# Kernel tuning notes

Hardware: AMD Instinct MI355X
Metric: run time of the kernel (lower is better)

Reference implementation:

```python
import jax, jax.numpy as jnp
import numpy as np

BN = 1024      # B*N voxel groups
M = 32         # points per voxel
D_MODEL = 128
D_POINTS = 64


def _mlp(x, w1, b1, w2, b2):
    # Linear -> ReLU -> Linear (torch nn.Sequential equivalent)
    return jax.nn.relu(x @ w1 + b1) @ w2 + b2


def setup_inputs() -> dict:
    key = jax.random.key(0)
    ks = jax.random.split(key, 16)
    def lin(k, din, dout):
        return (jax.random.normal(k, (din, dout), jnp.float32) / np.sqrt(din)).astype(jnp.float32)
    inp = {}
    inp["pv_xyz"] = jax.random.normal(ks[0], (BN, M, 3), jnp.float32)
    inp["features"] = jax.random.normal(ks[1], (BN, M, D_POINTS), jnp.float32)
    i = 2
    for name, din in [("alpha", 3), ("beta", 3), ("delta", 3), ("epsilon", D_MODEL), ("omega", D_POINTS)]:
        inp[f"{name}_w1"] = lin(ks[i], din, D_MODEL); i += 1
        inp[f"{name}_b1"] = jnp.zeros((D_MODEL,), jnp.float32)
        inp[f"{name}_w2"] = lin(ks[i], D_MODEL, D_MODEL); i += 1
        inp[f"{name}_b2"] = jnp.zeros((D_MODEL,), jnp.float32)
    return inp


def reference(pv_xyz, features,
              alpha_w1, alpha_b1, alpha_w2, alpha_b2,
              beta_w1, beta_b1, beta_w2, beta_b2,
              delta_w1, delta_b1, delta_w2, delta_b2,
              epsilon_w1, epsilon_b1, epsilon_w2, epsilon_b2,
              omega_w1, omega_b1, omega_w2, omega_b2):
    # abs relative position: [BN, M, M, 3]
    dist = jnp.abs(pv_xyz[:, :, None, :] - pv_xyz[:, None, :, :])
    pij = _mlp(dist, delta_w1, delta_b1, delta_w2, delta_b2)          # [BN,M,M,D]
    q = _mlp(pv_xyz, alpha_w1, alpha_b1, alpha_w2, alpha_b2)          # [BN,M,D]
    k = _mlp(pv_xyz, beta_w1, beta_b1, beta_w2, beta_b2)              # [BN,M,D]
    v = _mlp(features, omega_w1, omega_b1, omega_w2, omega_b2)        # [BN,M,D]
    scale = jnp.float32(1.0 / np.sqrt(D_MODEL))
    w = _mlp((q[:, :, None, :] - k[:, None, :, :] + pij) * scale,
             epsilon_w1, epsilon_b1, epsilon_w2, epsilon_b2)          # [BN,M,M,D]
    wij = jax.nn.softmax(w, axis=-2)                                  # softmax over key axis
    # torch.einsum('bmmf,bmf->bmf', wij, v): repeated index -> diagonal of wij
    midx = jnp.arange(wij.shape[1])
    res = wij[:, midx, midx, :] * v                                   # [BN,M,D]
    return jnp.concatenate([res, features], axis=-1)                  # [BN,M,D+C]
```

## Files before the change

### kernel.cpp

```cpp
#include <hip/hip_runtime.h>
#include <hip/hip_bf16.h>
#include <cstdint>
#include <cstddef>


#define SCALE 0.08838834764831843f
#define LOG2E 1.4426950408889634f

typedef __bf16 bf16x8 __attribute__((ext_vector_type(8)));
typedef float f32x16 __attribute__((ext_vector_type(16)));
typedef unsigned int u32x2 __attribute__((ext_vector_type(2)));

__device__ __forceinline__ ushort f2b(float f){
  __hip_bfloat16 h = __float2bfloat16(f);
  return __builtin_bit_cast(ushort, h);
}
__device__ __forceinline__ float b2f(uint32_t s){
  union { uint32_t u; float f; } x; x.u = s << 16; return x.f;
}
__device__ __forceinline__ float blo(uint32_t u){
  union { uint32_t x; float f; } v; v.x = u << 16; return v.f;
}
__device__ __forceinline__ float bhi(uint32_t u){
  union { uint32_t x; float f; } v; v.x = u & 0xffff0000u; return v.f;
}
__device__ __forceinline__ uint32_t pk2(float a, float b){
  union { __hip_bfloat162 h2; uint32_t u; } x;
  x.h2.x = __float2bfloat16(a); x.h2.y = __float2bfloat16(b);
  return x.u;
}
__device__ __forceinline__ f32x16 MFMA(uint4 a, uint4 b, f32x16 c){
  return __builtin_amdgcn_mfma_f32_32x32x16_bf16(
      __builtin_bit_cast(bf16x8, a), __builtin_bit_cast(bf16x8, b), c, 0, 0, 0);
}

__device__ __forceinline__ uint2 pswap(uint32_t a, uint32_t b){
#if __has_builtin(__builtin_amdgcn_permlane32_swap)
  u32x2 r = __builtin_amdgcn_permlane32_swap(a, b, false, false);
  uint2 o; o.x = r[0]; o.y = r[1]; return o;
#else
  uint32_t am = (uint32_t)__shfl_xor((int)a, 32);
  uint32_t bm = (uint32_t)__shfl_xor((int)b, 32);
  bool hi = (threadIdx.x & 32) != 0;
  uint2 o; o.x = hi ? bm : a; o.y = hi ? b : am; return o;
#endif
}

__device__ __forceinline__ void packswap(const f32x16 c, uint4& f0, uint4& f1){
  uint32_t p01 = pk2(fmaxf(c[0],0.f),  fmaxf(c[1],0.f));
  uint32_t p23 = pk2(fmaxf(c[2],0.f),  fmaxf(c[3],0.f));
  uint32_t p45 = pk2(fmaxf(c[4],0.f),  fmaxf(c[5],0.f));
  uint32_t p67 = pk2(fmaxf(c[6],0.f),  fmaxf(c[7],0.f));
  uint32_t p89 = pk2(fmaxf(c[8],0.f),  fmaxf(c[9],0.f));
  uint32_t pab = pk2(fmaxf(c[10],0.f), fmaxf(c[11],0.f));
  uint32_t pcd = pk2(fmaxf(c[12],0.f), fmaxf(c[13],0.f));
  uint32_t pef = pk2(fmaxf(c[14],0.f), fmaxf(c[15],0.f));
  uint2 s0 = pswap(p01, p45), s1 = pswap(p23, p67);
  uint2 s2 = pswap(p89, pcd), s3 = pswap(pab, pef);
  f0.x = s0.x; f0.y = s1.x; f0.z = s0.y; f0.w = s1.y;
  f1.x = s2.x; f1.y = s3.x; f1.z = s2.y; f1.w = s3.y;
}

__global__ __launch_bounds__(256) void k_pre(
    const float* __restrict__ A2, const float* __restrict__ B2, const float* __restrict__ D2,
    const float* __restrict__ E1, const float* __restrict__ E2,
    const float* __restrict__ O1, const float* __restrict__ O2,
    const float* __restrict__ ab2, const float* __restrict__ bb2, const float* __restrict__ db2,
    const float* __restrict__ eb1,
    const float* __restrict__ D1, const float* __restrict__ db1,
    ushort* __restrict__ aep, ushort* __restrict__ bep, ushort* __restrict__ gtp,
    ushort* __restrict__ e2p, ushort* __restrict__ o2p, ushort* __restrict__ o1t,
    ushort* __restrict__ d1p, float* __restrict__ c0)
{
  const int bid = blockIdx.x, tid = threadIdx.x;
  if (bid < 192){
    const float* W = (bid < 64) ? A2 : (bid < 128) ? B2 : D2;
    ushort* dst    = (bid < 64) ? aep : (bid < 128) ? bep : gtp;
    int flat = (bid & 63)*256 + tid;
    int co = flat >> 10, rem = flat & 1023, h = rem >> 3, i = rem & 7;
    int r = co*8 + i;
    float acc = 0.f;
    for (int t = 0; t < 128; ++t) acc = fmaf(W[r*128 + t], E1[t*128 + h], acc);
    dst[(co*128 + h)*8 + i] = f2b(acc * SCALE);
  } else if (bid < 256){
    int flat = (bid - 192)*256 + tid;
    int co = flat >> 10, rem = flat & 1023, d = rem >> 3, i = rem & 7;
    e2p[(co*128 + d)*8 + i] = f2b(E2[(co*8 + i)*128 + d] * LOG2E);
  } else if (bid < 320){
    int flat = (bid - 256)*256 + tid;
    int co = flat >> 10, rem = flat & 1023, d = rem >> 3, i = rem & 7;
    o2p[(co*128 + d)*8 + i] = f2b(O2[(co*8 + i)*128 + d]);
  } else if (bid < 352){
    int flat = (bid - 320)*256 + tid;
    int fo = flat >> 10, rem = flat & 1023, o = rem >> 3, e = rem & 7;
    o1t[(fo*128 + o)*8 + e] = f2b(O1[(fo*8 + e)*128 + o]);
  } else if (bid < 360){
    int flat = (bid - 352)*256 + tid;
    int koct = flat >> 10, cd = (flat >> 3) & 127, e = flat & 7;
    float val = 0.f;
    if (koct == 0){
      if (e < 3) val = D1[e*128 + cd];
      else if (e == 3) val = db1[cd];
    }
    d1p[flat] = f2b(val);
  } else {
    if (tid < 128){
      float acc = 0.f;
      for (int t = 0; t < 128; ++t) acc = fmaf(ab2[t] - bb2[t] + db2[t], E1[t*128 + tid], acc);
      c0[tid] = acc * SCALE + eb1[tid];
    }
  }
}

__device__ __forceinline__ void gemm64x128(const ushort (*sa)[64][8], const ushort (*sw)[128][8],
                                           int w, int l31, int hl, int p0,
                                           const float* __restrict__ bias,
                                           ushort* __restrict__ dst)
{
  const int rw = w >> 1, ctb = (w & 1) * 2;
  f32x16 acc0, acc1;
#pragma unroll
  for (int r = 0; r < 16; ++r){ acc0[r] = 0.f; acc1[r] = 0.f; }
#pragma unroll
  for (int kk = 0; kk < 8; ++kk){
    uint4 a  = *(const uint4*)&sa[2*kk + hl][32*rw + l31][0];
    uint4 b0 = *(const uint4*)&sw[2*kk + hl][32*ctb + l31][0];
    uint4 b1 = *(const uint4*)&sw[2*kk + hl][32*(ctb+1) + l31][0];
    acc0 = MFMA(a, b0, acc0);
    acc1 = MFMA(a, b1, acc1);
  }
#pragma unroll
  for (int t = 0; t < 2; ++t){
    const f32x16 acc = t ? acc1 : acc0;
    const int d = 32*(ctb + t) + l31;
    const float bv = bias ? bias[d] : 0.f;
#pragma unroll
    for (int r = 0; r < 16; ++r){
      int row = 32*rw + (r & 3) + 8*(r >> 2) + 4*hl;
      dst[(size_t)(p0 + row)*128 + d] = f2b(acc[r] + bv);
    }
  }
}

__global__ __launch_bounds__(256, 2) void k_point(
    const float* __restrict__ pv, const float* __restrict__ feat,
    const float* __restrict__ A1, const float* __restrict__ ab1,
    const float* __restrict__ B1, const float* __restrict__ bb1,
    const float* __restrict__ ob1, const float* __restrict__ ob2,
    const float* __restrict__ c0,
    const uint4* __restrict__ aep, const uint4* __restrict__ bep,
    const uint4* __restrict__ o1t, const uint4* __restrict__ o2p,
    ushort* __restrict__ qe_ws, ushort* __restrict__ ke_ws, ushort* __restrict__ v_ws,
    float* __restrict__ out)
{
  __shared__ ushort sW[16][128][8];
  __shared__ ushort sA[16][64][8];
  __shared__ ushort sF[8][64][8];
  __shared__ float  sLw[3][128];
  __shared__ float  sLb[128];
  __shared__ float  sLb2[128];

  const int tid = threadIdx.x;
  const int p0  = blockIdx.x * 64;
  const int w = tid >> 6, lane = tid & 63, l31 = lane & 31, hl = lane >> 5;

  for (int idx = tid; idx < 64*16; idx += 256){
    int p = idx >> 4, k4 = idx & 15;
    float4 f = ((const float4*)(feat + (size_t)(p0 + p)*64))[k4];
    ((float4*)(out + (size_t)(p0 + p)*192 + 128))[k4] = f;
  }

  for (int idx = tid; idx < 2048; idx += 256) ((uint4*)sW)[idx] = aep[idx];
  for (int idx = tid; idx < 384; idx += 256) ((float*)sLw)[idx] = A1[idx];
  if (tid < 128) sLb[tid] = ab1[tid];
  __syncthreads();
  {
    int p = tid & 63, ob = tid >> 6;
    float x0 = pv[(size_t)(p0+p)*3+0], x1 = pv[(size_t)(p0+p)*3+1], x2 = pv[(size_t)(p0+p)*3+2];
#pragma unroll
    for (int it = 0; it < 4; ++it){
      int oct = ob + 4*it;
      float h[8];
#pragma unroll
      for (int e = 0; e < 8; ++e){
        int cd = oct*8 + e;
        float t = fmaf(x0, sLw[0][cd], fmaf(x1, sLw[1][cd], fmaf(x2, sLw[2][cd], sLb[cd])));
        h[e] = fmaxf(t, 0.f);
      }
      uint4 u; u.x = pk2(h[0],h[1]); u.y = pk2(h[2],h[3]); u.z = pk2(h[4],h[5]); u.w = pk2(h[6],h[7]);
      *(uint4*)&sA[oct][p][0] = u;
    }
  }
  __syncthreads();
  gemm64x128(sA, sW, w, l31, hl, p0, c0, qe_ws);
  __syncthreads();

  for (int idx = tid; idx < 2048; idx += 256) ((uint4*)sW)[idx] = bep[idx];
  for (int idx = tid; idx < 384; idx += 256) ((float*)sLw)[idx] = B1[idx];
  if (tid < 128) sLb[tid] = bb1[tid];
  __syncthreads();
  {
    int p = tid & 63, ob = tid >> 6;
    float x0 = pv[(size_t)(p0+p)*3+0], x1 = pv[(size_t)(p0+p)*3+1], x2 = pv[(size_t)(p0+p)*3+2];
#pragma unroll
    for (int it = 0; it < 4; ++it){
      int oct = ob + 4*it;
      float h[8];
#pragma unroll
      for (int e = 0; e < 8; ++e){
        int cd = oct*8 + e;
        float t = fmaf(x0, sLw[0][cd], fmaf(x1, sLw[1][cd], fmaf(x2, sLw[2][cd], sLb[cd])));
        h[e] = fmaxf(t, 0.f);
      }
      uint4 u; u.x = pk2(h[0],h[1]); u.y = pk2(h[2],h[3]); u.z = pk2(h[4],h[5]); u.w = pk2(h[6],h[7]);
      *(uint4*)&sA[oct][p][0] = u;
    }
  }
  __syncthreads();
  gemm64x128(sA, sW, w, l31, hl, p0, nullptr, ke_ws);
  __syncthreads();

  for (int idx = tid; idx < 512; idx += 256){
    int p = idx & 63, fo = idx >> 6;
    const float* fp = feat + (size_t)(p0 + p)*64 + 8*fo;
    float4 f0 = ((const float4*)fp)[0], f1 = ((const float4*)fp)[1];
    uint4 u; u.x = pk2(f0.x,f0.y); u.y = pk2(f0.z,f0.w); u.z = pk2(f1.x,f1.y); u.w = pk2(f1.z,f1.w);
    *(uint4*)&sF[fo][p][0] = u;
  }
  for (int idx = tid; idx < 1024; idx += 256) ((uint4*)sW)[idx] = o1t[idx];
  if (tid < 128) sLb[tid] = ob1[tid];
  __syncthreads();
  {
    f32x16 acc0, acc1;
#pragma unroll
    for (int r = 0; r < 16; ++r){ acc0[r] = 0.f; acc1[r] = 0.f; }
#pragma unroll
    for (int kk = 0; kk < 4; ++kk){
      uint4 a  = *(const uint4*)&sW[2*kk + hl][32*w + l31][0];
      uint4 b0 = *(const uint4*)&sF[2*kk + hl][l31][0];
      uint4 b1 = *(const uint4*)&sF[2*kk + hl][32 + l31][0];
      acc0 = MFMA(a, b0, acc0);
      acc1 = MFMA(a, b1, acc1);
    }
#pragma unroll
    for (int t = 0; t < 2; ++t){
      const f32x16 acc = t ? acc1 : acc0;
      const int pt = 32*t + l31;
#pragma unroll
      for (int q = 0; q < 4; ++q){
        int o0 = 32*w + 8*q + 4*hl;
        float z0 = fmaxf(acc[4*q+0] + sLb[o0+0], 0.f);
        float z1 = fmaxf(acc[4*q+1] + sLb[o0+1], 0.f);
        float z2 = fmaxf(acc[4*q+2] + sLb[o0+2], 0.f);
        float z3 = fmaxf(acc[4*q+3] + sLb[o0+3], 0.f);
        uint2 u; u.x = pk2(z0, z1); u.y = pk2(z2, z3);
        *(uint2*)&sA[4*w + q][pt][4*hl] = u;
      }
    }
  }
  __syncthreads();

  for (int idx = tid; idx < 2048; idx += 256) ((uint4*)sW)[idx] = o2p[idx];
  if (tid < 128) sLb2[tid] = ob2[tid];
  __syncthreads();
  {
    const int rw = w >> 1, ctb = (w & 1) * 2;
    f32x16 acc0, acc1;
#pragma unroll
    for (int r = 0; r < 16; ++r){ acc0[r] = 0.f; acc1[r] = 0.f; }
#pragma unroll
    for (int kk = 0; kk < 8; ++kk){
      uint4 a  = *(const uint4*)&sA[2*kk + hl][32*rw + l31][0];
      uint4 b0 = *(const uint4*)&sW[2*kk + hl][32*ctb + l31][0];
      uint4 b1 = *(const uint4*)&sW[2*kk + hl][32*(ctb+1) + l31][0];
      acc0 = MFMA(a, b0, acc0);
      acc1 = MFMA(a, b1, acc1);
    }
#pragma unroll
    for (int t = 0; t < 2; ++t){
      const f32x16 acc = t ? acc1 : acc0;
      const int d = 32*(ctb + t) + l31;
      const float bias = sLb2[d];
#pragma unroll
      for (int r = 0; r < 16; ++r){
        int row = 32*rw + (r & 3) + 8*(r >> 2) + 4*hl;
        v_ws[(size_t)(p0 + row)*128 + d] = f2b(acc[r] + bias);
      }
    }
  }
}

__global__ __launch_bounds__(256, 2) void k_main(
    const float* __restrict__ pv,
    const ushort* __restrict__ qe_ws, const ushort* __restrict__ ke_ws, const ushort* __restrict__ v_ws,
    const uint4* __restrict__ gtp, const uint4* __restrict__ e2p, const uint4* __restrict__ d1p,
    float* __restrict__ out)
{
  __shared__ uint4 sG[2048];
  __shared__ uint4 sE[2048];
  __shared__ uint2 sK[1024];
  __shared__ float sXYZ[32][3];

  const int tid = threadIdx.x;
  const int b = blockIdx.x;
  const int w = tid >> 6, lane = tid & 63, l31 = lane & 31, hl = lane >> 5;

  for (int idx = tid; idx < 2048; idx += 256){ sG[idx] = gtp[idx]; sE[idx] = e2p[idx]; }
  for (int idx = tid; idx < 1024; idx += 256){
    int j = idx & 31, rest = idx >> 5;
    int khl = rest & 1, slot = rest >> 1;
    int h0 = 32*(slot >> 2) + 8*(slot & 3) + 4*khl;
    sK[idx] = *(const uint2*)(ke_ws + (size_t)(b*32 + j)*128 + h0);
  }
  for (int idx = tid; idx < 96; idx += 256) ((float*)sXYZ)[idx] = pv[(size_t)b*96 + idx];

  uint4 wD[4];
#pragma unroll
  for (int t = 0; t < 4; ++t) wD[t] = d1p[hl*128 + 32*t + l31];
  f32x16 ZERO;
#pragma unroll
  for (int r = 0; r < 16; ++r) ZERO[r] = 0.f;
  __syncthreads();

  const float xj0 = sXYZ[l31][0], xj1 = sXYZ[l31][1], xj2 = sXYZ[l31][2];
  const ushort* qbase = qe_ws + (size_t)b*32*128;

#pragma unroll
  for (int pp = 0; pp < 4; ++pp){
    const int i0 = 8*w + 2*pp, i1 = i0 + 1;

    uint4 bDa, bDb;
    {
      float a0 = sXYZ[i0][0], a1 = sXYZ[i0][1], a2 = sXYZ[i0][2];
      float c0_ = sXYZ[i1][0], c1_ = sXYZ[i1][1], c2_ = sXYZ[i1][2];
      bDa.x = pk2(fabsf(a0-xj0), fabsf(a1-xj1)); bDa.y = pk2(fabsf(a2-xj2), 1.0f);
      bDa.z = 0u; bDa.w = 0u;
      bDb.x = pk2(fabsf(c0_-xj0), fabsf(c1_-xj1)); bDb.y = pk2(fabsf(c2_-xj2), 1.0f);
      bDb.z = 0u; bDb.w = 0u;
    }

    uint4 hdA[8], hdB[8];
#pragma unroll
    for (int t = 0; t < 4; ++t){
      f32x16 ca = MFMA(wD[t], bDa, ZERO);
      f32x16 cb = MFMA(wD[t], bDb, ZERO);
      packswap(ca, hdA[2*t], hdA[2*t+1]);
      packswap(cb, hdB[2*t], hdB[2*t+1]);
    }

    uint4 heA[8], heB[8];
#pragma unroll
    for (int t = 0; t < 4; ++t){
      f32x16 aA, aB;
#pragma unroll
      for (int q = 0; q < 4; ++q){
        uint2 kq = sK[((t*4 + q)*2 + hl)*32 + l31];
        uint2 qa = *(const uint2*)(qbase + (size_t)i0*128 + 32*t + 8*q + 4*hl);
        uint2 qb = *(const uint2*)(qbase + (size_t)i1*128 + 32*t + 8*q + 4*hl);
        float k0 = blo(kq.x), k1 = bhi(kq.x), k2 = blo(kq.y), k3 = bhi(kq.y);
        aA[4*q+0] = blo(qa.x) - k0; aA[4*q+1] = bhi(qa.x) - k1;
        aA[4*q+2] = blo(qa.y) - k2; aA[4*q+3] = bhi(qa.y) - k3;
        aB[4*q+0] = blo(qb.x) - k0; aB[4*q+1] = bhi(qb.x) - k1;
        aB[4*q+2] = blo(qb.y) - k2; aB[4*q+3] = bhi(qb.y) - k3;
      }
#pragma unroll
      for (int kk = 0; kk < 8; ++kk){
        uint4 wg = sG[(2*kk + hl)*128 + 32*t + l31];
        aA = MFMA(wg, hdA[kk], aA);
        aB = MFMA(wg, hdB[kk], aB);
      }
      packswap(aA, heA[2*t], heA[2*t+1]);
      packswap(aB, heB[2*t], heB[2*t+1]);
    }

    const int rl   = (2*pp) & 3;
    const int hsel = pp >> 1;
#pragma unroll
    for (int t = 0; t < 4; ++t){
      float va = b2f((uint32_t)v_ws[(size_t)(b*32 + i0)*128 + 32*t + l31]);
      float vb = b2f((uint32_t)v_ws[(size_t)(b*32 + i1)*128 + 32*t + l31]);
      f32x16 cA, cB;
#pragma unroll
      for (int kk = 0; kk < 8; ++kk){
        uint4 we = sE[(2*kk + hl)*128 + 32*t + l31];
        cA = MFMA(heA[kk], we, kk ? cA : ZERO);
        cB = MFMA(heB[kk], we, kk ? cB : ZERO);
      }
#pragma unroll
      for (int r = 0; r < 16; ++r) cA[r] = __builtin_amdgcn_exp2f(cA[r]);
#pragma unroll
      for (int r = 0; r < 16; ++r) cB[r] = __builtin_amdgcn_exp2f(cB[r]);
      float sA = ((cA[0]+cA[1])+(cA[2]+cA[3])) + ((cA[4]+cA[5])+(cA[6]+cA[7]))
               + ((cA[8]+cA[9])+(cA[10]+cA[11])) + ((cA[12]+cA[13])+(cA[14]+cA[15]));
      float sB = ((cB[0]+cB[1])+(cB[2]+cB[3])) + ((cB[4]+cB[5])+(cB[6]+cB[7]))
               + ((cB[8]+cB[9])+(cB[10]+cB[11])) + ((cB[12]+cB[13])+(cB[14]+cB[15]));
      uint2 swA = pswap(__builtin_bit_cast(uint32_t, sA), __builtin_bit_cast(uint32_t, sA));
      uint2 swB = pswap(__builtin_bit_cast(uint32_t, sB), __builtin_bit_cast(uint32_t, sB));
      float sAt = __builtin_bit_cast(float, swA.x) + __builtin_bit_cast(float, swA.y);
      float sBt = __builtin_bit_cast(float, swB.x) + __builtin_bit_cast(float, swB.y);
      float nA = (w == 0) ? cA[rl]   : (w == 1) ? cA[rl+4]   : (w == 2) ? cA[rl+8]   : cA[rl+12];
      float nB = (w == 0) ? cB[rl+1] : (w == 1) ? cB[rl+5]   : (w == 2) ? cB[rl+9]   : cB[rl+13];
      if (hl == hsel){
        out[(size_t)(b*32 + i0)*192 + 32*t + l31] = nA * __builtin_amdgcn_rcpf(sAt) * va;
        out[(size_t)(b*32 + i1)*192 + 32*t + l31] = nB * __builtin_amdgcn_rcpf(sBt) * vb;
      }
    }
  }
}

static constexpr size_t OFF_AEP = 0;
static constexpr size_t OFF_BEP = 32768;
static constexpr size_t OFF_GTP = 65536;
static constexpr size_t OFF_E2P = 98304;
static constexpr size_t OFF_O1T = 131072;
static constexpr size_t OFF_O2P = 147456;
static constexpr size_t OFF_C0  = 180224;
static constexpr size_t OFF_D1P = 180736;
static constexpr size_t OFF_QE  = 184832;
static constexpr size_t OFF_KE  = OFF_QE + (size_t)32768*128*2;
static constexpr size_t OFF_V   = OFF_KE + (size_t)32768*128*2;

extern "C" void kernel_launch(void* const* d_in, const int* in_sizes, int n_in,
                              void* d_out, int out_size, void* d_ws, size_t ws_size,
                              hipStream_t stream)
{
  (void)in_sizes; (void)n_in; (void)out_size; (void)ws_size;
  const float* pv   = (const float*)d_in[0];
  const float* feat = (const float*)d_in[1];
  const float* A1 = (const float*)d_in[2];  const float* ab1 = (const float*)d_in[3];
  const float* A2 = (const float*)d_in[4];  const float* ab2 = (const float*)d_in[5];
  const float* B1 = (const float*)d_in[6];  const float* bb1 = (const float*)d_in[7];
  const float* B2 = (const float*)d_in[8];  const float* bb2 = (const float*)d_in[9];
  const float* D1 = (const float*)d_in[10]; const float* db1 = (const float*)d_in[11];
  const float* D2 = (const float*)d_in[12]; const float* db2 = (const float*)d_in[13];
  const float* E1 = (const float*)d_in[14]; const float* eb1 = (const float*)d_in[15];
  const float* E2 = (const float*)d_in[16];
  const float* O1 = (const float*)d_in[18]; const float* ob1 = (const float*)d_in[19];
  const float* O2 = (const float*)d_in[20]; const float* ob2 = (const float*)d_in[21];

  char* ws = (char*)d_ws;
  ushort* aep = (ushort*)(ws + OFF_AEP);
  ushort* bep = (ushort*)(ws + OFF_BEP);
  ushort* gtp = (ushort*)(ws + OFF_GTP);
  ushort* e2p = (ushort*)(ws + OFF_E2P);
  ushort* o1t = (ushort*)(ws + OFF_O1T);
  ushort* o2p = (ushort*)(ws + OFF_O2P);
  float*  c0  = (float*)(ws + OFF_C0);
  ushort* d1p = (ushort*)(ws + OFF_D1P);
  ushort* qe  = (ushort*)(ws + OFF_QE);
  ushort* ke  = (ushort*)(ws + OFF_KE);
  ushort* vv  = (ushort*)(ws + OFF_V);
  float* out = (float*)d_out;

  hipLaunchKernelGGL(k_pre, dim3(361), dim3(256), 0, stream,
                     A2, B2, D2, E1, E2, O1, O2, ab2, bb2, db2, eb1, D1, db1,
                     aep, bep, gtp, e2p, o2p, o1t, d1p, c0);
  hipLaunchKernelGGL(k_point, dim3(512), dim3(256), 0, stream,
                     pv, feat, A1, ab1, B1, bb1, ob1, ob2, c0,
                     (const uint4*)aep, (const uint4*)bep, (const uint4*)o1t, (const uint4*)o2p,
                     qe, ke, vv, out);
  hipLaunchKernelGGL(k_main, dim3(1024), dim3(256), 0, stream,
                     pv, qe, ke, vv, (const uint4*)gtp, (const uint4*)e2p, (const uint4*)d1p,
                     out);
}
```

Measured before the change: 120.1 us.

## Drop shared gamma weights, read them from global, process one row at a time

```diff
diff --git a/kernel.cpp b/kernel.cpp
--- a/kernel.cpp
+++ b/kernel.cpp
@@ -296,7 +296,6 @@
     const uint4* __restrict__ gtp, const uint4* __restrict__ e2p, const uint4* __restrict__ d1p,
     float* __restrict__ out)
 {
-  __shared__ uint4 sG[2048];
   __shared__ uint4 sE[2048];
   __shared__ uint2 sK[1024];
   __shared__ float sXYZ[32][3];
@@ -305,7 +304,7 @@
   const int b = blockIdx.x;
   const int w = tid >> 6, lane = tid & 63, l31 = lane & 31, hl = lane >> 5;
 
-  for (int idx = tid; idx < 2048; idx += 256){ sG[idx] = gtp[idx]; sE[idx] = e2p[idx]; }
+  for (int idx = tid; idx < 2048; idx += 256) sE[idx] = e2p[idx];
   for (int idx = tid; idx < 1024; idx += 256){
     int j = idx & 31, rest = idx >> 5;
     int khl = rest & 1, slot = rest >> 1;
@@ -324,85 +323,71 @@
 
   const float xj0 = sXYZ[l31][0], xj1 = sXYZ[l31][1], xj2 = sXYZ[l31][2];
   const ushort* qbase = qe_ws + (size_t)b*32*128;
-
-#pragma unroll
-  for (int pp = 0; pp < 4; ++pp){
-    const int i0 = 8*w + 2*pp, i1 = i0 + 1;
-
-    uint4 bDa, bDb;
-    {
-      float a0 = sXYZ[i0][0], a1 = sXYZ[i0][1], a2 = sXYZ[i0][2];
-      float c0_ = sXYZ[i1][0], c1_ = sXYZ[i1][1], c2_ = sXYZ[i1][2];
-      bDa.x = pk2(fabsf(a0-xj0), fabsf(a1-xj1)); bDa.y = pk2(fabsf(a2-xj2), 1.0f);
-      bDa.z = 0u; bDa.w = 0u;
-      bDb.x = pk2(fabsf(c0_-xj0), fabsf(c1_-xj1)); bDb.y = pk2(fabsf(c2_-xj2), 1.0f);
-      bDb.z = 0u; bDb.w = 0u;
-    }
-
-    uint4 hdA[8], hdB[8];
-#pragma unroll
-    for (int t = 0; t < 4; ++t){
-      f32x16 ca = MFMA(wD[t], bDa, ZERO);
-      f32x16 cb = MFMA(wD[t], bDb, ZERO);
-      packswap(ca, hdA[2*t], hdA[2*t+1]);
-      packswap(cb, hdB[2*t], hdB[2*t+1]);
-    }
-
-    uint4 heA[8], heB[8];
-#pragma unroll
-    for (int t = 0; t < 4; ++t){
-      f32x16 aA, aB;
-#pragma unroll
-      for (int q = 0; q < 4; ++q){
-        uint2 kq = sK[((t*4 + q)*2 + hl)*32 + l31];
-        uint2 qa = *(const uint2*)(qbase + (size_t)i0*128 + 32*t + 8*q + 4*hl);
-        uint2 qb = *(const uint2*)(qbase + (size_t)i1*128 + 32*t + 8*q + 4*hl);
-        float k0 = blo(kq.x), k1 = bhi(kq.x), k2 = blo(kq.y), k3 = bhi(kq.y);
-        aA[4*q+0] = blo(qa.x) - k0; aA[4*q+1] = bhi(qa.x) - k1;
-        aA[4*q+2] = blo(qa.y) - k2; aA[4*q+3] = bhi(qa.y) - k3;
-        aB[4*q+0] = blo(qb.x) - k0; aB[4*q+1] = bhi(qb.x) - k1;
-        aB[4*q+2] = blo(qb.y) - k2; aB[4*q+3] = bhi(qb.y) - k3;
-      }
-#pragma unroll
-      for (int kk = 0; kk < 8; ++kk){
-        uint4 wg = sG[(2*kk + hl)*128 + 32*t + l31];
-        aA = MFMA(wg, hdA[kk], aA);
-        aB = MFMA(wg, hdB[kk], aB);
-      }
-      packswap(aA, heA[2*t], heA[2*t+1]);
-      packswap(aB, heB[2*t], heB[2*t+1]);
-    }
-
-    const int rl   = (2*pp) & 3;
-    const int hsel = pp >> 1;
-#pragma unroll
-    for (int t = 0; t < 4; ++t){
-      float va = b2f((uint32_t)v_ws[(size_t)(b*32 + i0)*128 + 32*t + l31]);
-      float vb = b2f((uint32_t)v_ws[(size_t)(b*32 + i1)*128 + 32*t + l31]);
-      f32x16 cA, cB;
-#pragma unroll
-      for (int kk = 0; kk < 8; ++kk){
-        uint4 we = sE[(2*kk + hl)*128 + 32*t + l31];
-        cA = MFMA(heA[kk], we, kk ? cA : ZERO);
-        cB = MFMA(heB[kk], we, kk ? cB : ZERO);
-      }
-#pragma unroll
-      for (int r = 0; r < 16; ++r) cA[r] = __builtin_amdgcn_exp2f(cA[r]);
-#pragma unroll
-      for (int r = 0; r < 16; ++r) cB[r] = __builtin_amdgcn_exp2f(cB[r]);
-      float sA = ((cA[0]+cA[1])+(cA[2]+cA[3])) + ((cA[4]+cA[5])+(cA[6]+cA[7]))
-               + ((cA[8]+cA[9])+(cA[10]+cA[11])) + ((cA[12]+cA[13])+(cA[14]+cA[15]));
-      float sB = ((cB[0]+cB[1])+(cB[2]+cB[3])) + ((cB[4]+cB[5])+(cB[6]+cB[7]))
-               + ((cB[8]+cB[9])+(cB[10]+cB[11])) + ((cB[12]+cB[13])+(cB[14]+cB[15]));
-      uint2 swA = pswap(__builtin_bit_cast(uint32_t, sA), __builtin_bit_cast(uint32_t, sA));
-      uint2 swB = pswap(__builtin_bit_cast(uint32_t, sB), __builtin_bit_cast(uint32_t, sB));
-      float sAt = __builtin_bit_cast(float, swA.x) + __builtin_bit_cast(float, swA.y);
-      float sBt = __builtin_bit_cast(float, swB.x) + __builtin_bit_cast(float, swB.y);
-      float nA = (w == 0) ? cA[rl]   : (w == 1) ? cA[rl+4]   : (w == 2) ? cA[rl+8]   : cA[rl+12];
-      float nB = (w == 0) ? cB[rl+1] : (w == 1) ? cB[rl+5]   : (w == 2) ? cB[rl+9]   : cB[rl+13];
-      if (hl == hsel){
-        out[(size_t)(b*32 + i0)*192 + 32*t + l31] = nA * __builtin_amdgcn_rcpf(sAt) * va;
-        out[(size_t)(b*32 + i1)*192 + 32*t + l31] = nB * __builtin_amdgcn_rcpf(sBt) * vb;
+  const uint4* gbase = gtp + hl*128 + l31;
+
+#pragma unroll
+  for (int ro = 0; ro < 2; ++ro){
+#pragma unroll
+    for (int ri = 0; ri < 4; ++ri){
+      const int rr = 4*ro + ri;
+      const int i = 8*w + rr;
+
+      uint4 bD;
+      {
+        float a0 = sXYZ[i][0], a1 = sXYZ[i][1], a2 = sXYZ[i][2];
+        bD.x = pk2(fabsf(a0-xj0), fabsf(a1-xj1)); bD.y = pk2(fabsf(a2-xj2), 1.0f);
+        bD.z = 0u; bD.w = 0u;
+      }
+
+      uint4 hd[8];
+#pragma unroll
+      for (int t = 0; t < 4; ++t){
+        f32x16 c = MFMA(wD[t], bD, ZERO);
+        packswap(c, hd[2*t], hd[2*t+1]);
+      }
+
+      uint4 he[8];
+#pragma unroll
+      for (int t = 0; t < 4; ++t){
+        f32x16 a;
+#pragma unroll
+        for (int q = 0; q < 4; ++q){
+          uint2 kq = sK[((t*4 + q)*2 + hl)*32 + l31];
+          uint2 qa = *(const uint2*)(qbase + (size_t)i*128 + 32*t + 8*q + 4*hl);
+          a[4*q+0] = blo(qa.x) - blo(kq.x);
+          a[4*q+1] = bhi(qa.x) - bhi(kq.x);
+          a[4*q+2] = blo(qa.y) - blo(kq.y);
+          a[4*q+3] = bhi(qa.y) - bhi(kq.y);
+        }
+#pragma unroll
+        for (int kk = 0; kk < 8; ++kk){
+          uint4 wg = gbase[kk*256 + 32*t];
+          a = MFMA(wg, hd[kk], a);
+        }
+        packswap(a, he[2*t], he[2*t+1]);
+      }
+
+      const int rl   = rr & 3;
+      const int hsel = (rr >> 2) & 1;
+#pragma unroll
+      for (int t = 0; t < 4; ++t){
+        float va = b2f((uint32_t)v_ws[(size_t)(b*32 + i)*128 + 32*t + l31]);
+        f32x16 c;
+#pragma unroll
+        for (int kk = 0; kk < 8; ++kk){
+          uint4 we = sE[(2*kk + hl)*128 + 32*t + l31];
+          c = MFMA(he[kk], we, kk ? c : ZERO);
+        }
+#pragma unroll
+        for (int r = 0; r < 16; ++r) c[r] = __builtin_amdgcn_exp2f(c[r]);
+        float s = ((c[0]+c[1])+(c[2]+c[3])) + ((c[4]+c[5])+(c[6]+c[7]))
+                + ((c[8]+c[9])+(c[10]+c[11])) + ((c[12]+c[13])+(c[14]+c[15]));
+        uint2 sw = pswap(__builtin_bit_cast(uint32_t, s), __builtin_bit_cast(uint32_t, s));
+        float st = __builtin_bit_cast(float, sw.x) + __builtin_bit_cast(float, sw.y);
+        float n = (w == 0) ? c[rl] : (w == 1) ? c[rl+4] : (w == 2) ? c[rl+8] : c[rl+12];
+        if (hl == hsel){
+          out[(size_t)(b*32 + i)*192 + 32*t + l31] = n * __builtin_amdgcn_rcpf(st) * va;
+        }
       }
     }
   }
```

After: 171.8 us. 1.43x slower.
